# Kernel optimization log

Measured on AMD Instinct MI355X. Metric: run time of the kernel, lower is better.

Reference implementation:

```python
import jax, jax.numpy as jnp
import numpy as np

C_DIM = 128
HIDDEN = 128
RESO = 128
PADDING = 0.1


def _resnet_block(x, w0, b0, w1, b1, ws):
    # ResnetBlockFC: net = fc_0(relu(x)); dx = fc_1(relu(net)); out = shortcut(x) + dx
    net = jnp.maximum(x, 0.0) @ w0 + b0
    dx = jnp.maximum(net, 0.0) @ w1 + b1
    return x @ ws + dx


def _scatter_mean(c, index, num_seg):
    # c: (B, T, C) float, index: (B, T) int -> (B, num_seg, C), empty bins stay 0
    def one(cb, ib):
        s = jax.ops.segment_sum(cb, ib, num_segments=num_seg)
        cnt = jax.ops.segment_sum(jnp.ones((cb.shape[0],), cb.dtype), ib, num_segments=num_seg)
        return s / jnp.maximum(cnt, 1.0)[:, None]
    return jax.vmap(one)(c, index)


def setup_inputs() -> dict:
    key = jax.random.key(0)
    ks = jax.random.split(key, 12)
    B, T, D = 2, 65536, 3
    h = HIDDEN
    p = jax.random.uniform(ks[0], (B, T, D), jnp.float32, minval=-0.5, maxval=0.5)
    s = 0.02
    fc_pos_w = jax.random.normal(ks[1], (D, 2 * h), jnp.float32) * s
    fc_pos_b = jax.random.normal(ks[2], (2 * h,), jnp.float32) * s
    # 5 ResnetBlockFC blocks, all (2h -> h) since c_dim == hidden_dim
    w0 = jax.random.normal(ks[3], (5, 2 * h, h), jnp.float32) * s
    b0 = jax.random.normal(ks[4], (5, h), jnp.float32) * s
    w1 = jax.random.normal(ks[5], (5, h, h), jnp.float32) * s
    b1 = jax.random.normal(ks[6], (5, h), jnp.float32) * s
    ws = jax.random.normal(ks[7], (5, 2 * h, h), jnp.float32) * s  # shortcut, no bias
    return {"p": p, "fc_pos_w": fc_pos_w, "fc_pos_b": fc_pos_b,
            "w0": w0, "b0": b0, "w1": w1, "b1": b1, "ws": ws}


def reference(p, fc_pos_w, fc_pos_b, w0, b0, w1, b1, ws):
    # PointNet ResNet encoder
    net = p @ fc_pos_w + fc_pos_b  # (B, T, 2h)
    for i in range(5):
        hfeat = _resnet_block(net, w0[i], b0[i], w1[i], b1[i], ws[i])  # (B, T, h)
        if i < 4:
            pooled = jnp.max(hfeat, axis=1, keepdims=True)
            net = jnp.concatenate([hfeat, jnp.broadcast_to(pooled, hfeat.shape)], axis=-1)
    c = hfeat  # (B, T, c_dim)

    # normalize_coordinate(plane='xz'): take dims (0, 2), map to [0, 1)
    xy = p[..., jnp.array([0, 2])]
    xy = xy / (1.0 + PADDING + 1e-3) + 0.5
    xy = jnp.clip(xy, 0.0, 1.0 - 1e-6)
    # coordinate2index
    xi = (xy * RESO).astype(jnp.int32)
    index = xi[..., 0] + RESO * xi[..., 1]  # (B, T)

    fea = _scatter_mean(c, index, RESO * RESO)  # (B, R*R, c_dim)
    fea_plane = jnp.transpose(fea, (0, 2, 1)).reshape(p.shape[0], C_DIM, RESO, RESO)
    return fea_plane
```

## Files before the change

kernel.cpp:

```cpp
#include <hip/hip_runtime.h>
#include <hip/hip_bf16.h>


#define G_ALL 131072
#define HD    128
#define NBINS 16384

typedef __attribute__((ext_vector_type(8))) short short8;
typedef __attribute__((ext_vector_type(4))) float f32x4;

#define MFMA16(a, b, c) __builtin_amdgcn_mfma_f32_16x16x32_bf16(a, b, c, 0, 0, 0)

__device__ __forceinline__ float bf16_to_f32(unsigned short u) {
  union { unsigned int u; float f; } v; v.u = ((unsigned int)u) << 16; return v.f;
}
__device__ __forceinline__ unsigned short f32_to_bf16(float f) {
  union { float f; unsigned int u; } v; v.f = f;
  unsigned int u = v.u;
  u += 0x7fffu + ((u >> 16) & 1u);
  return (unsigned short)(u >> 16);
}
__device__ __forceinline__ unsigned int f32_key(float f) {
  union { float f; unsigned int u; } v; v.f = f;
  return (v.u & 0x80000000u) ? ~v.u : (v.u | 0x80000000u);
}
__device__ __forceinline__ float key_f32(unsigned int k) {
  union { unsigned int u; float f; } v;
  v.u = (k & 0x80000000u) ? (k & 0x7fffffffu) : ~k;
  return v.f;
}
__device__ __forceinline__ int bin_of(float p0, float p2) {
  float x = p0 / 1.101f + 0.5f;
  x = fminf(fmaxf(x, 0.0f), 1.0f - 1e-6f);
  int xi = (int)(x * 128.0f);
  float z = p2 / 1.101f + 0.5f;
  z = fminf(fmaxf(z, 0.0f), 1.0f - 1e-6f);
  int zi = (int)(z * 128.0f);
  return xi + 128 * zi;
}
__device__ __forceinline__ short8 relu8(short8 a) {
  short8 r;
#pragma unroll
  for (int e = 0; e < 8; e++) r[e] = a[e] < 0 ? (short)0 : a[e];
  return r;
}

__global__ void prep_kernel(const float* __restrict__ fcw,
                            const float* __restrict__ fcb,
                            const float* __restrict__ ws0,
                            float* __restrict__ Sp, float* __restrict__ bsp,
                            unsigned int* __restrict__ pool,
                            int* __restrict__ hist) {
  int j = threadIdx.x;
  for (int d = 0; d < 3; d++) {
    float s = 0.f;
    for (int ch = 0; ch < 256; ch++)
      s = fmaf(fcw[d * 256 + ch], ws0[ch * HD + j], s);
    Sp[d * HD + j] = s;
  }
  float s = 0.f;
  for (int ch = 0; ch < 256; ch++)
    s = fmaf(fcb[ch], ws0[ch * HD + j], s);
  bsp[j] = s;
  for (int k = j; k < 4 * 2 * 128; k += 128) pool[k] = 0u;
  for (int k = j; k < 2 * NBINS; k += 128) hist[k] = 0;
}

__global__ void wprep_kernel(const float* __restrict__ w0,
                             const float* __restrict__ w1,
                             const float* __restrict__ ws,
                             unsigned short* __restrict__ B0t,
                             unsigned short* __restrict__ W0t,
                             unsigned short* __restrict__ W1t,
                             unsigned short* __restrict__ WSt) {
  int gid = blockIdx.x * 256 + threadIdx.x;
  float v;
  unsigned short* dstp;
  int dst;
  if (gid < 32768) {
    int n = gid >> 8, k = gid & 255;
    v = w0[k * 128 + n];
    dstp = B0t; dst = gid;
  } else if (gid < 98304) {
    int i = gid - 32768; int s = i >> 14; int n = (i >> 7) & 127; int k = i & 127;
    v = w0[(size_t)((s + 1) * 256 + k) * 128 + n];
    dstp = W0t; dst = i;
  } else if (gid < 180224) {
    int i = gid - 98304; int s = i >> 14; int n = (i >> 7) & 127; int k = i & 127;
    v = w1[(size_t)(s * 128 + k) * 128 + n];
    dstp = W1t; dst = i;
  } else if (gid < 245760) {
    int i = gid - 180224; int s = i >> 14; int n = (i >> 7) & 127; int k = i & 127;
    v = ws[(size_t)((s + 1) * 256 + k) * 128 + n];
    dstp = WSt; dst = i;
  } else return;
  dstp[dst] = f32_to_bf16(v);
}

__global__ __launch_bounds__(256) void index_kernel(const float* __restrict__ p,
                                                    int* __restrict__ hist) {
  int g = blockIdx.x * 256 + threadIdx.x;
  int b = g >> 16;
  int idx = bin_of(p[3 * (size_t)g], p[3 * (size_t)g + 2]);
  atomicAdd(&hist[b * NBINS + idx], 1);
}

__global__ __launch_bounds__(1024) void scan_kernel(int* __restrict__ hist,
                                                    int* __restrict__ offsets) {
  __shared__ int sd[1024];
  int t = threadIdx.x;
  int vals[32];
  int s = 0;
#pragma unroll
  for (int i = 0; i < 32; i++) { vals[i] = hist[t * 32 + i]; s += vals[i]; }
  sd[t] = s;
  __syncthreads();
  for (int d = 1; d < 1024; d <<= 1) {
    int v = (t >= d) ? sd[t - d] : 0;
    __syncthreads();
    sd[t] += v;
    __syncthreads();
  }
  int run = sd[t] - s;
#pragma unroll
  for (int i = 0; i < 32; i++) {
    offsets[t * 32 + i] = run;
    hist[t * 32 + i] = run;
    run += vals[i];
  }
  if (t == 1023) offsets[32768] = run;
}

__global__ __launch_bounds__(256) void fill_kernel(const float* __restrict__ p,
                                                   int* __restrict__ cursor,
                                                   int* __restrict__ order) {
  int g = blockIdx.x * 256 + threadIdx.x;
  int b = g >> 16;
  int idx = bin_of(p[3 * (size_t)g], p[3 * (size_t)g + 2]);
  int pos = atomicAdd(&cursor[b * NBINS + idx], 1);
  order[pos] = g;
}

__global__ __launch_bounds__(256) void gather_kernel(
    const unsigned short* __restrict__ c, const int* __restrict__ offsets,
    const int* __restrict__ order, float* __restrict__ out) {
  int wave = threadIdx.x >> 6, lane = threadIdx.x & 63;
  int b = blockIdx.x >> 8;
  int binBase = (blockIdx.x & 255) * 64 + wave * 16;
  for (int bi = 0; bi < 16; bi++) {
    int B = b * NBINS + binBase + bi;
    int st = offsets[B], en = offsets[B + 1];
    float a0 = 0.f, a1 = 0.f;
    for (int k = st; k < en; k++) {
      int g = order[k];
      unsigned int u = *(const unsigned int*)(c + (size_t)g * HD + lane * 2);
      a0 += bf16_to_f32((unsigned short)(u & 0xffffu));
      a1 += bf16_to_f32((unsigned short)(u >> 16));
    }
    float cf = fmaxf((float)(en - st), 1.0f);
    size_t base = (size_t)b * HD * NBINS + (size_t)(binBase + bi);
    out[base + (size_t)(2 * lane) * NBINS] = a0 / cf;
    out[base + (size_t)(2 * lane + 1) * NBINS] = a1 / cf;
  }
}

__global__ __launch_bounds__(512, 4) void stage0_kernel(
    const float* __restrict__ p, const float* __restrict__ fcw,
    const float* __restrict__ fcb,
    const unsigned short* __restrict__ B0t,
    const unsigned short* __restrict__ W1t,
    const float* __restrict__ b0, const float* __restrict__ b1,
    const float* __restrict__ Sp, const float* __restrict__ bsp,
    unsigned short* __restrict__ hout, unsigned int* __restrict__ pool) {
  __shared__ float fcL[1024];
  __shared__ float ptL[64 * 5];
  __shared__ unsigned short x0t[64 * 264];
  __shared__ unsigned short m2[64 * 136];
  const int tid = threadIdx.x;
  const int lane = tid & 63;
  const int q = lane >> 4, l15 = lane & 15;
  const int nt = tid >> 6;
  const int b = blockIdx.x >> 8;
  const int wrow = nt * 16 + l15;

  short8 b0w[8], w1w[4];
#pragma unroll
  for (int kc = 0; kc < 8; kc++)
    b0w[kc] = *(const short8*)(B0t + (size_t)wrow * 256 + kc * 32 + q * 8);
#pragma unroll
  for (int kc = 0; kc < 4; kc++)
    w1w[kc] = *(const short8*)(W1t + (size_t)wrow * 128 + kc * 32 + q * 8);
  const float bias1 = b0[wrow];
  const float bias2 = bsp[wrow] + b1[wrow];
  const float sp0 = Sp[wrow], sp1 = Sp[128 + wrow], sp2 = Sp[256 + wrow];

  for (int k = tid; k < 1024; k += 512)
    fcL[k] = (k < 768) ? fcw[k] : fcb[k - 768];

  for (int it = 0; it < 4; it++) {
    const int rowBase = (blockIdx.x * 4 + it) * 64;
    __syncthreads();
    if (tid < 192) ptL[(tid / 3) * 5 + (tid % 3)] = p[(size_t)rowBase * 3 + tid];
    {
      int row = tid >> 3, c8 = tid & 7;
      const float* pr = p + (size_t)(rowBase + row) * 3;
      float p0 = pr[0], p1 = pr[1], p2 = pr[2];
#pragma unroll
      for (int cc = 0; cc < 32; cc++) {
        int ch = c8 + cc * 8;
        float x = fcL[768 + ch] + p0 * fcL[ch] + p1 * fcL[256 + ch] + p2 * fcL[512 + ch];
        x0t[row * 264 + ch] = f32_to_bf16(fmaxf(x, 0.f));
      }
    }
    __syncthreads();
    f32x4 C1[4];
#pragma unroll
    for (int s = 0; s < 4; s++) C1[s] = (f32x4){bias1, bias1, bias1, bias1};
#pragma unroll
    for (int kc = 0; kc < 8; kc++) {
#pragma unroll
      for (int s = 0; s < 4; s++) {
        short8 Ar = *(const short8*)(&x0t[(s * 16 + l15) * 264 + kc * 32 + q * 8]);
        C1[s] = MFMA16(Ar, b0w[kc], C1[s]);
      }
    }
#pragma unroll
    for (int s = 0; s < 4; s++)
#pragma unroll
      for (int r = 0; r < 4; r++)
        m2[(s * 16 + q * 4 + r) * 136 + nt * 16 + l15] =
            f32_to_bf16(fmaxf(C1[s][r], 0.f));
    __syncthreads();
    f32x4 C2[4];
#pragma unroll
    for (int s = 0; s < 4; s++)
#pragma unroll
      for (int r = 0; r < 4; r++) {
        int row = s * 16 + q * 4 + r;
        C2[s][r] = bias2 + ptL[row * 5] * sp0 + ptL[row * 5 + 1] * sp1 +
                   ptL[row * 5 + 2] * sp2;
      }
#pragma unroll
    for (int kc = 0; kc < 4; kc++) {
#pragma unroll
      for (int s = 0; s < 4; s++) {
        short8 Am = *(const short8*)(&m2[(s * 16 + l15) * 136 + kc * 32 + q * 8]);
        C2[s] = MFMA16(Am, w1w[kc], C2[s]);
      }
    }
#pragma unroll
    for (int s = 0; s < 4; s++)
#pragma unroll
      for (int r = 0; r < 4; r++)
        x0t[(s * 16 + q * 4 + r) * 136 + nt * 16 + l15] = f32_to_bf16(C2[s][r]);
    {
      float m = -1e30f;
#pragma unroll
      for (int s = 0; s < 4; s++)
#pragma unroll
        for (int r = 0; r < 4; r++) m = fmaxf(m, C2[s][r]);
      m = fmaxf(m, __shfl_xor(m, 16, 64));
      m = fmaxf(m, __shfl_xor(m, 32, 64));
      if (lane < 16) atomicMax(&pool[b * 128 + nt * 16 + lane], f32_key(m));
    }
    __syncthreads();
    {
      int r = tid >> 3, cs = (tid & 7) * 16;
      short8 v0 = *(const short8*)(&x0t[r * 136 + cs]);
      short8 v1 = *(const short8*)(&x0t[r * 136 + cs + 8]);
      *(short8*)(hout + (size_t)(rowBase + r) * 128 + cs) = v0;
      *(short8*)(hout + (size_t)(rowBase + r) * 128 + cs + 8) = v1;
    }
  }
}

__global__ __launch_bounds__(512, 4) void stageN_kernel(
    const unsigned short* __restrict__ hin, unsigned short* __restrict__ hout,
    const unsigned short* __restrict__ W0t,
    const unsigned short* __restrict__ W1t,
    const unsigned short* __restrict__ WSt,
    const float* __restrict__ b0e, const float* __restrict__ bse,
    unsigned int* __restrict__ pool, int doPool) {
  __shared__ unsigned short At[64 * 136];
  __shared__ unsigned short m2[64 * 136];
  const int tid = threadIdx.x;
  const int lane = tid & 63;
  const int q = lane >> 4, l15 = lane & 15;
  const int nt = tid >> 6;
  const int b = blockIdx.x >> 8;
  const int wrow = nt * 16 + l15;

  short8 w0w[4], w1w[4], wsw[4];
#pragma unroll
  for (int kc = 0; kc < 4; kc++) {
    w0w[kc] = *(const short8*)(W0t + (size_t)wrow * 128 + kc * 32 + q * 8);
    w1w[kc] = *(const short8*)(W1t + (size_t)wrow * 128 + kc * 32 + q * 8);
    wsw[kc] = *(const short8*)(WSt + (size_t)wrow * 128 + kc * 32 + q * 8);
  }
  const float bias1 = b0e[b * 128 + wrow];
  const float bias2 = bse[b * 128 + wrow];
  const int r8 = tid >> 3, cs8 = (tid & 7) * 16;

  for (int it = 0; it < 4; it++) {
    const int rowBase = (blockIdx.x * 4 + it) * 64;
    __syncthreads();
    {
      const size_t gb = ((size_t)rowBase + r8) * 128 + cs8;
      short8 v0 = *(const short8*)(hin + gb);
      short8 v1 = *(const short8*)(hin + gb + 8);
      *(short8*)(&At[r8 * 136 + cs8]) = v0;
      *(short8*)(&At[r8 * 136 + cs8 + 8]) = v1;
    }
    __syncthreads();
    f32x4 C1[4], C2[4];
#pragma unroll
    for (int s = 0; s < 4; s++) {
      C1[s] = (f32x4){bias1, bias1, bias1, bias1};
      C2[s] = (f32x4){bias2, bias2, bias2, bias2};
    }
#pragma unroll
    for (int kc = 0; kc < 4; kc++) {
#pragma unroll
      for (int s = 0; s < 4; s++) {
        short8 Ah = *(const short8*)(&At[(s * 16 + l15) * 136 + kc * 32 + q * 8]);
        short8 Ar = relu8(Ah);
        C1[s] = MFMA16(Ar, w0w[kc], C1[s]);
        C2[s] = MFMA16(Ah, wsw[kc], C2[s]);
      }
    }
#pragma unroll
    for (int s = 0; s < 4; s++)
#pragma unroll
      for (int r = 0; r < 4; r++)
        m2[(s * 16 + q * 4 + r) * 136 + nt * 16 + l15] =
            f32_to_bf16(fmaxf(C1[s][r], 0.f));
    __syncthreads();
#pragma unroll
    for (int kc = 0; kc < 4; kc++) {
#pragma unroll
      for (int s = 0; s < 4; s++) {
        short8 Am = *(const short8*)(&m2[(s * 16 + l15) * 136 + kc * 32 + q * 8]);
        C2[s] = MFMA16(Am, w1w[kc], C2[s]);
      }
    }
    if (doPool) {
      float m = -1e30f;
#pragma unroll
      for (int s = 0; s < 4; s++)
#pragma unroll
        for (int r = 0; r < 4; r++) m = fmaxf(m, C2[s][r]);
      m = fmaxf(m, __shfl_xor(m, 16, 64));
      m = fmaxf(m, __shfl_xor(m, 32, 64));
      if (lane < 16) atomicMax(&pool[b * 128 + nt * 16 + lane], f32_key(m));
    }
    __syncthreads();
#pragma unroll
    for (int s = 0; s < 4; s++)
#pragma unroll
      for (int r = 0; r < 4; r++)
        m2[(s * 16 + q * 4 + r) * 136 + nt * 16 + l15] = f32_to_bf16(C2[s][r]);
    __syncthreads();
    {
      short8 v0 = *(const short8*)(&m2[r8 * 136 + cs8]);
      short8 v1 = *(const short8*)(&m2[r8 * 136 + cs8 + 8]);
      *(short8*)(hout + (size_t)(rowBase + r8) * 128 + cs8) = v0;
      *(short8*)(hout + (size_t)(rowBase + r8) * 128 + cs8 + 8) = v1;
    }
  }
}

__global__ void fold_kernel(const unsigned int* __restrict__ pool,
                            const float* __restrict__ b0s,
                            const float* __restrict__ b1s,
                            const float* __restrict__ w0hi,
                            const float* __restrict__ wshi,
                            float* __restrict__ b0e, float* __restrict__ bse) {
  __shared__ float ps[256];
  int tid = threadIdx.x;
  int b = tid >> 7, j = tid & 127;
  ps[tid] = key_f32(pool[tid]);
  __syncthreads();
  float a0 = b0s[j], a1 = b1s[j];
  for (int ch = 0; ch < 128; ch++) {
    float pv = ps[b * 128 + ch];
    a0 = fmaf(fmaxf(pv, 0.f), w0hi[ch * HD + j], a0);
    a1 = fmaf(pv, wshi[ch * HD + j], a1);
  }
  b0e[b * 128 + j] = a0;
  bse[b * 128 + j] = a1;
}

extern "C" void kernel_launch(void* const* d_in, const int* in_sizes, int n_in,
                              void* d_out, int out_size, void* d_ws,
                              size_t ws_size, hipStream_t stream) {
  const float* p   = (const float*)d_in[0];
  const float* fcw = (const float*)d_in[1];
  const float* fcb = (const float*)d_in[2];
  const float* w0  = (const float*)d_in[3];
  const float* b0  = (const float*)d_in[4];
  const float* w1  = (const float*)d_in[5];
  const float* b1  = (const float*)d_in[6];
  const float* wsc = (const float*)d_in[7];
  float* out = (float*)d_out;

  char* wsp = (char*)d_ws;
  unsigned short* hA = (unsigned short*)wsp;
  unsigned short* hB = hA + (size_t)G_ALL * HD;
  unsigned short* B0t = hB + (size_t)G_ALL * HD;
  unsigned short* W0t = B0t + 32768;
  unsigned short* W1t = W0t + 65536;
  unsigned short* WSt = W1t + 81920;
  unsigned int* pool = (unsigned int*)(WSt + 65536);
  float* b0e = (float*)(pool + 1024);
  float* bse = b0e + 1024;
  float* Sp  = bse + 1024;
  float* bsp = Sp + 384;
  int* hist    = (int*)(bsp + 128);
  int* offsets = hist + 2 * NBINS;
  int* order   = offsets + 2 * NBINS + 4;

  prep_kernel<<<1, 128, 0, stream>>>(fcw, fcb, wsc, Sp, bsp, pool, hist);
  wprep_kernel<<<960, 256, 0, stream>>>(w0, w1, wsc, B0t, W0t, W1t, WSt);
  index_kernel<<<512, 256, 0, stream>>>(p, hist);
  scan_kernel<<<1, 1024, 0, stream>>>(hist, offsets);
  fill_kernel<<<512, 256, 0, stream>>>(p, hist, order);

  stage0_kernel<<<512, 512, 0, stream>>>(p, fcw, fcb, B0t, W1t,
                                         b0, b1, Sp, bsp, hA, pool);
  unsigned short* hin = hA;
  unsigned short* hout = hB;
  for (int s = 1; s < 5; s++) {
    fold_kernel<<<1, 256, 0, stream>>>(
        pool + (s - 1) * 256, b0 + s * HD, b1 + s * HD,
        w0 + (size_t)(s * 256 + 128) * HD, wsc + (size_t)(s * 256 + 128) * HD,
        b0e + (s - 1) * 256, bse + (s - 1) * 256);
    stageN_kernel<<<512, 512, 0, stream>>>(
        hin, hout, W0t + (s - 1) * 16384, W1t + s * 16384,
        WSt + (s - 1) * 16384, b0e + (s - 1) * 256, bse + (s - 1) * 256,
        pool + s * 256, (s < 4) ? 1 : 0);
    unsigned short* t = hin; hin = hout; hout = t;
  }
  gather_kernel<<<512, 256, 0, stream>>>(hin, offsets, order, out);
}
```

Before: 390.9 us.

## Fuse pooled-bias fold into stage kernels and stage gather output via LDS

Removes the single-block fold_kernel launches and has every stageN block recompute the pooled-feature bias fold itself, adding bias after the MFMA accumulation instead of seeding it. The gather kernel now accumulates per-bin sums into a shared-memory tile and writes the channel-major output with coalesced stores instead of strided scattered writes. This saves four serial tiny launches and improves output write coalescing, at the cost of redundant 128-step fold loops per block.

```diff
diff --git a/kernel.cpp b/kernel.cpp
--- a/kernel.cpp
+++ b/kernel.cpp
@@ -144,12 +144,19 @@
 __global__ __launch_bounds__(256) void gather_kernel(
     const unsigned short* __restrict__ c, const int* __restrict__ offsets,
     const int* __restrict__ order, float* __restrict__ out) {
-  int wave = threadIdx.x >> 6, lane = threadIdx.x & 63;
-  int b = blockIdx.x >> 8;
-  int binBase = (blockIdx.x & 255) * 64 + wave * 16;
+  __shared__ float acc[129 * 65];
+  const int tid = threadIdx.x;
+  const int wave = tid >> 6, lane = tid & 63;
+  const int B0 = blockIdx.x * 64;
+  const int b = B0 >> 14;
+
+  for (int i = tid; i < 129 * 65; i += 256) acc[i] = 0.f;
+  __syncthreads();
+
   for (int bi = 0; bi < 16; bi++) {
-    int B = b * NBINS + binBase + bi;
-    int st = offsets[B], en = offsets[B + 1];
+    const int binL = wave * 16 + bi;
+    const int B = B0 + binL;
+    const int st = offsets[B], en = offsets[B + 1];
     float a0 = 0.f, a1 = 0.f;
     for (int k = st; k < en; k++) {
       int g = order[k];
@@ -157,10 +164,18 @@
       a0 += bf16_to_f32((unsigned short)(u & 0xffffu));
       a1 += bf16_to_f32((unsigned short)(u >> 16));
     }
-    float cf = fmaxf((float)(en - st), 1.0f);
-    size_t base = (size_t)b * HD * NBINS + (size_t)(binBase + bi);
-    out[base + (size_t)(2 * lane) * NBINS] = a0 / cf;
-    out[base + (size_t)(2 * lane + 1) * NBINS] = a1 / cf;
+    acc[(2 * lane) * 65 + binL] = a0;
+    acc[(2 * lane + 1) * 65 + binL] = a1;
+    if (lane == 0) acc[128 * 65 + binL] = (float)(en - st);
+  }
+  __syncthreads();
+
+  const size_t outBase = (size_t)b * HD * NBINS + (size_t)(B0 & (NBINS - 1));
+  const float cnt = fmaxf(acc[128 * 65 + lane], 1.0f);
+#pragma unroll
+  for (int c2 = 0; c2 < 32; c2++) {
+    int ch = wave * 32 + c2;
+    out[outBase + (size_t)ch * NBINS + lane] = acc[ch * 65 + lane] / cnt;
   }
 }
 
@@ -279,7 +294,10 @@
     const unsigned short* __restrict__ W0t,
     const unsigned short* __restrict__ W1t,
     const unsigned short* __restrict__ WSt,
-    const float* __restrict__ b0e, const float* __restrict__ bse,
+    const unsigned int* __restrict__ poolPrev,
+    const float* __restrict__ b0s, const float* __restrict__ b1s,
+    const float* __restrict__ w0hi,
+    const float* __restrict__ wshi,
     unsigned int* __restrict__ pool, int doPool) {
   __shared__ unsigned short At[64 * 136];
   __shared__ unsigned short m2[64 * 136];
@@ -297,8 +315,12 @@
     w1w[kc] = *(const short8*)(W1t + (size_t)wrow * 128 + kc * 32 + q * 8);
     wsw[kc] = *(const short8*)(WSt + (size_t)wrow * 128 + kc * 32 + q * 8);
   }
-  const float bias1 = b0e[b * 128 + wrow];
-  const float bias2 = bse[b * 128 + wrow];
+  float bias1 = b0s[wrow], bias2 = b1s[wrow];
+  for (int ch = 0; ch < 128; ch++) {
+    float pv = key_f32(poolPrev[b * 128 + ch]);
+    bias1 = fmaf(fmaxf(pv, 0.f), w0hi[ch * HD + wrow], bias1);
+    bias2 = fmaf(pv, wshi[ch * HD + wrow], bias2);
+  }
   const int r8 = tid >> 3, cs8 = (tid & 7) * 16;
 
   for (int it = 0; it < 4; it++) {
@@ -315,8 +337,8 @@
     f32x4 C1[4], C2[4];
 #pragma unroll
     for (int s = 0; s < 4; s++) {
-      C1[s] = (f32x4){bias1, bias1, bias1, bias1};
-      C2[s] = (f32x4){bias2, bias2, bias2, bias2};
+      C1[s] = (f32x4){0.f, 0.f, 0.f, 0.f};
+      C2[s] = (f32x4){0.f, 0.f, 0.f, 0.f};
     }
 #pragma unroll
     for (int kc = 0; kc < 4; kc++) {
@@ -333,7 +355,7 @@
 #pragma unroll
       for (int r = 0; r < 4; r++)
         m2[(s * 16 + q * 4 + r) * 136 + nt * 16 + l15] =
-            f32_to_bf16(fmaxf(C1[s][r], 0.f));
+            f32_to_bf16(fmaxf(C1[s][r] + bias1, 0.f));
     __syncthreads();
 #pragma unroll
     for (int kc = 0; kc < 4; kc++) {
@@ -343,6 +365,10 @@
         C2[s] = MFMA16(Am, w1w[kc], C2[s]);
       }
     }
+#pragma unroll
+    for (int s = 0; s < 4; s++)
+#pragma unroll
+      for (int r = 0; r < 4; r++) C2[s][r] += bias2;
     if (doPool) {
       float m = -1e30f;
 #pragma unroll
@@ -367,27 +393,6 @@
       *(short8*)(hout + (size_t)(rowBase + r8) * 128 + cs8 + 8) = v1;
     }
   }
-}
-
-__global__ void fold_kernel(const unsigned int* __restrict__ pool,
-                            const float* __restrict__ b0s,
-                            const float* __restrict__ b1s,
-                            const float* __restrict__ w0hi,
-                            const float* __restrict__ wshi,
-                            float* __restrict__ b0e, float* __restrict__ bse) {
-  __shared__ float ps[256];
-  int tid = threadIdx.x;
-  int b = tid >> 7, j = tid & 127;
-  ps[tid] = key_f32(pool[tid]);
-  __syncthreads();
-  float a0 = b0s[j], a1 = b1s[j];
-  for (int ch = 0; ch < 128; ch++) {
-    float pv = ps[b * 128 + ch];
-    a0 = fmaf(fmaxf(pv, 0.f), w0hi[ch * HD + j], a0);
-    a1 = fmaf(pv, wshi[ch * HD + j], a1);
-  }
-  b0e[b * 128 + j] = a0;
-  bse[b * 128 + j] = a1;
 }
 
 extern "C" void kernel_launch(void* const* d_in, const int* in_sizes, int n_in,
@@ -411,9 +416,7 @@
   unsigned short* W1t = W0t + 65536;
   unsigned short* WSt = W1t + 81920;
   unsigned int* pool = (unsigned int*)(WSt + 65536);
-  float* b0e = (float*)(pool + 1024);
-  float* bse = b0e + 1024;
-  float* Sp  = bse + 1024;
+  float* Sp  = (float*)(pool + 1024);
   float* bsp = Sp + 384;
   int* hist    = (int*)(bsp + 128);
   int* offsets = hist + 2 * NBINS;
@@ -430,13 +433,11 @@
   unsigned short* hin = hA;
   unsigned short* hout = hB;
   for (int s = 1; s < 5; s++) {
-    fold_kernel<<<1, 256, 0, stream>>>(
-        pool + (s - 1) * 256, b0 + s * HD, b1 + s * HD,
-        w0 + (size_t)(s * 256 + 128) * HD, wsc + (size_t)(s * 256 + 128) * HD,
-        b0e + (s - 1) * 256, bse + (s - 1) * 256);
     stageN_kernel<<<512, 512, 0, stream>>>(
         hin, hout, W0t + (s - 1) * 16384, W1t + s * 16384,
-        WSt + (s - 1) * 16384, b0e + (s - 1) * 256, bse + (s - 1) * 256,
+        WSt + (s - 1) * 16384, pool + (s - 1) * 256,
+        b0 + s * HD, b1 + s * HD,
+        w0 + (size_t)(s * 256 + 128) * HD, wsc + (size_t)(s * 256 + 128) * HD,
         pool + s * 256, (s < 4) ? 1 : 0);
     unsigned short* t = hin; hin = hout; hout = t;
   }
```

Result: slower. 457.3 us (+17.0%).
